# Optimization experiments

Measured on AMD Instinct MI355X. Metric: run time of the kernel, lower is better.

## Reference

```python
import jax, jax.numpy as jnp
import numpy as np

D_MODEL = 2048
B, L = 4, 2048


def _dwconv(x, w, b):
    # x: (B, D, L), w: (D, 1, 3), b: (D,). Causal depthwise conv (PyTorch pad=2 then [...,:L]).
    y = jax.lax.conv_general_dilated(
        x, w, window_strides=(1,), padding=[(2, 0)],
        feature_group_count=x.shape[1], dimension_numbers=("NCH", "OIH", "NCH"))
    return y + b[None, :, None]


def setup_inputs() -> dict:
    key = jax.random.key(0)
    ks = jax.random.split(key, 12)
    D = D_MODEL
    s = 0.02
    inp = {
        "u": jax.random.normal(ks[0], (B, L, D), jnp.float32),
        "Wq": jax.random.normal(ks[1], (D, D), jnp.float32) * s,
        "bq": jnp.zeros((D,), jnp.float32),
        "Wk": jax.random.normal(ks[2], (D, D), jnp.float32) * s,
        "bk": jnp.zeros((D,), jnp.float32),
        "Wv": jax.random.normal(ks[3], (D, D), jnp.float32) * s,
        "bv": jnp.zeros((D,), jnp.float32),
        "convq_w": jax.random.normal(ks[4], (D, 1, 3), jnp.float32) * 0.5,
        "convq_b": jnp.zeros((D,), jnp.float32),
        "convk_w": jax.random.normal(ks[5], (D, 1, 3), jnp.float32) * 0.5,
        "convk_b": jnp.zeros((D,), jnp.float32),
        "ssm_kernel": jax.random.normal(ks[6], (D, L), jnp.float32) * 0.01,  # H = d_model (head_dim=1)
        "D_skip": jax.random.normal(ks[7], (D,), jnp.float32),
        "Wo": jax.random.normal(ks[8], (D, D), jnp.float32) * s,
        "bo": jnp.zeros((D,), jnp.float32),
    }
    return inp


def reference(u, Wq, bq, Wk, bk, Wv, bv, convq_w, convq_b, convk_w, convk_b,
              ssm_kernel, D_skip, Wo, bo):
    # u: (B, L, H)  head_dim = 1 so H == d_model
    Lq = u.shape[1]
    fft_size = 2 * Lq  # L_kernel + L with l_max=None, rate=1

    # q/k/v projections (W @ u.T + b in torch == u @ W.T + b)
    q = jnp.einsum("blh,eh->ble", u, Wq) + bq
    k = jnp.einsum("blh,eh->ble", u, Wk) + bk
    v = jnp.einsum("blh,eh->ble", u, Wv) + bv
    q = jnp.transpose(q, (0, 2, 1))  # (B, H, L)
    k = jnp.transpose(k, (0, 2, 1))
    v = jnp.transpose(v, (0, 2, 1))

    # causal depthwise short convs
    q = _dwconv(q, convq_w, convq_b)
    k = _dwconv(k, convk_w, convk_b)

    # head_dim = 1: kv outer product collapses to elementwise product (B, H, L)
    kv = k * v

    # FFT long convolution: torch does rfft(kv)/n * rfft(kernel), irfft norm='forward'
    # which equals the standard unnormalized circular conv below.
    kv_f = jnp.fft.rfft(kv, n=fft_size)
    kernel_f = jnp.fft.rfft(ssm_kernel, n=fft_size)  # (H, F)
    y = jnp.fft.irfft(kv_f * kernel_f, n=fft_size)[..., :Lq]

    # D skip and q gating
    y = (y + kv * D_skip[None, :, None]) * q  # (B, H, L)

    # output projection
    y = jnp.transpose(y, (0, 2, 1))  # (B, L, H)
    return jnp.einsum("blh,eh->ble", y, Wo) + bo
```

## Files before the change

### kernel.cpp

```cpp
#include <hip/hip_runtime.h>
#include <cstdint>
#include <cstddef>

#define DD 2048
#define LL 2048
#define BB 4
#define MM (BB * LL)
#define NN 6144

typedef __bf16 bf16;
typedef __bf16 bf16x8 __attribute__((ext_vector_type(8)));
typedef __bf16 bf16x4 __attribute__((ext_vector_type(4)));
typedef __bf16 bf16x2 __attribute__((ext_vector_type(2)));
typedef float f32x4 __attribute__((ext_vector_type(4)));

__device__ __forceinline__ void gload16(const void* g, void* l) {
    __builtin_amdgcn_global_load_lds(
        (const __attribute__((address_space(1))) void*)g,
        (__attribute__((address_space(3))) void*)l, 16, 0, 0);
}

__global__ __launch_bounds__(256) void cvt_f32_bf16(const float* __restrict__ s,
                                                    bf16* __restrict__ d, int n8) {
    int i = blockIdx.x * 256 + threadIdx.x;
    if (i >= n8) return;
    const float4* sp = (const float4*)s + (size_t)i * 2;
    float4 a = sp[0], b = sp[1];
    bf16x8 o;
    o[0] = (bf16)a.x; o[1] = (bf16)a.y; o[2] = (bf16)a.z; o[3] = (bf16)a.w;
    o[4] = (bf16)b.x; o[5] = (bf16)b.y; o[6] = (bf16)b.z; o[7] = (bf16)b.w;
    *((bf16x8*)d + i) = o;
}

__device__ __forceinline__ void stage_half(const bf16* g, bf16* l, size_t rstep, int tid) {
    gload16(g, l + tid * 8);
    gload16(g + rstep, l + 4096 + tid * 8);
}

#define MFMA16(J0, J1)                                                         \
    __builtin_amdgcn_s_setprio(1);                                             \
    _Pragma("unroll") for (int i = 0; i < 8; i++)                              \
        acc[i][J0] = __builtin_amdgcn_mfma_f32_16x16x32_bf16(af[i], bq[J0],    \
                                                             acc[i][J0], 0, 0, 0); \
    _Pragma("unroll") for (int i = 0; i < 8; i++)                              \
        acc[i][J1] = __builtin_amdgcn_mfma_f32_16x16x32_bf16(af[i], bq[J1],    \
                                                             acc[i][J1], 0, 0, 0); \
    __builtin_amdgcn_s_setprio(0);

template <int NT>
__device__ __forceinline__ void mma256_loop(const bf16* gA, const bf16* gB,
                                            int Kdim, bf16* lds,
                                            f32x4 (&acc)[8][4]) {
    const int tid = threadIdx.x;
    const int wave = tid >> 6, lane = tid & 63;
    const int wm = wave >> 2, wn = wave & 3;
    const int fm = lane & 15, fg = lane >> 4;
    const size_t rstep = (size_t)128 * Kdim;
    const int koff = ((fg ^ ((fm >> 1) & 3)) << 3);
    const int aoff = (wm * 128 + fm) * 32 + koff;
    const int boff = (wn * 64 + fm) * 32 + koff;

    bf16* const A0 = lds;
    bf16* const B0 = lds + 32768;

#pragma unroll
    for (int i = 0; i < 8; i++)
#pragma unroll
        for (int j = 0; j < 4; j++) acc[i][j] = (f32x4){0.f, 0.f, 0.f, 0.f};

    stage_half(gA, A0, rstep, tid);
    stage_half(gB, B0, rstep, tid);
    stage_half(gA + 32, A0 + 8192, rstep, tid);
    stage_half(gB + 32, B0 + 8192, rstep, tid);

    bf16x8 af[8], bq[4];

    for (int t = 0; t < NT; ++t) {
        const int c = t & 1;
        bf16* const Ac = A0 + c * 16384;
        bf16* const Bc = B0 + c * 16384;
        bf16* const An = A0 + (c ^ 1) * 16384;
        bf16* const Bn = B0 + (c ^ 1) * 16384;
        const bf16* a1 = gA + (t + 1) * 64;
        const bf16* b1 = gB + (t + 1) * 64;
        const bool st = (t + 1 < NT);

        asm volatile("s_waitcnt vmcnt(4)" ::: "memory");
        __builtin_amdgcn_s_barrier();
        if (st) stage_half(a1, An, rstep, tid);
#pragma unroll
        for (int i = 0; i < 8; i++) af[i] = *(const bf16x8*)(Ac + aoff + i * 512);
        bq[0] = *(const bf16x8*)(Bc + boff);
        bq[1] = *(const bf16x8*)(Bc + boff + 512);
        __builtin_amdgcn_s_barrier();
        asm volatile("s_waitcnt lgkmcnt(0)" ::: "memory");
        MFMA16(0, 1)

        __builtin_amdgcn_s_barrier();
        if (st) stage_half(b1, Bn, rstep, tid);
        bq[2] = *(const bf16x8*)(Bc + boff + 1024);
        bq[3] = *(const bf16x8*)(Bc + boff + 1536);
        __builtin_amdgcn_s_barrier();
        asm volatile("s_waitcnt lgkmcnt(0)" ::: "memory");
        MFMA16(2, 3)

        if (st) { asm volatile("s_waitcnt vmcnt(4)" ::: "memory"); }
        else    { asm volatile("s_waitcnt vmcnt(0)" ::: "memory"); }
        __builtin_amdgcn_s_barrier();
        if (st) stage_half(a1 + 32, An + 8192, rstep, tid);
#pragma unroll
        for (int i = 0; i < 8; i++) af[i] = *(const bf16x8*)(Ac + 8192 + aoff + i * 512);
        bq[0] = *(const bf16x8*)(Bc + 8192 + boff);
        bq[1] = *(const bf16x8*)(Bc + 8192 + boff + 512);
        __builtin_amdgcn_s_barrier();
        asm volatile("s_waitcnt lgkmcnt(0)" ::: "memory");
        MFMA16(0, 1)

        __builtin_amdgcn_s_barrier();
        if (st) stage_half(b1 + 32, Bn + 8192, rstep, tid);
        bq[2] = *(const bf16x8*)(Bc + 8192 + boff + 1024);
        bq[3] = *(const bf16x8*)(Bc + 8192 + boff + 1536);
        __builtin_amdgcn_s_barrier();
        asm volatile("s_waitcnt lgkmcnt(0)" ::: "memory");
        MFMA16(2, 3)
    }
}

__global__ __launch_bounds__(512, 2) void gemm_qkv(const bf16* __restrict__ A,
                                                   const bf16* __restrict__ Bm,
                                                   const float* __restrict__ bqp,
                                                   const float* __restrict__ bkp,
                                                   const float* __restrict__ bvp,
                                                   bf16* __restrict__ CtOut) {
    __shared__ bf16 lds[65536];
    const int id = blockIdx.x;
    const int wg = (id & 7) * 96 + (id >> 3);
    const int m0 = (wg & 31) << 8;
    const int n0 = (wg >> 5) << 8;

    const int tid = threadIdx.x;
    const int wave = tid >> 6, lane = tid & 63;
    const int srow = tid >> 2;
    const int skx = (((lane & 3) ^ ((lane >> 3) & 3)) << 3);
    const bf16* gA = A + (size_t)(m0 + srow) * DD + skx;
    const bf16* gB = Bm + (size_t)(n0 + srow) * DD + skx;

    f32x4 acc[8][4];
    mma256_loop<DD / 64>(gA, gB, DD, lds, acc);

    __syncthreads();
    const int wm = wave >> 2, wn = wave & 3;
    const int fm = lane & 15, fg = lane >> 4;
    const float* bp = (n0 < 2048) ? bqp : ((n0 < 4096) ? bkp : bvp);
    const int nb = n0 & 2047;
#pragma unroll
    for (int j = 0; j < 4; j++) {
        const int col = wn * 64 + j * 16 + fm;
        const float bvv = bp[nb + col];
        const int csw = (col & 7) << 3;
#pragma unroll
        for (int i = 0; i < 8; i++) {
            const int row = (wm * 128 + i * 16 + fg * 4) ^ csw;
            bf16x4 o;
#pragma unroll
            for (int r = 0; r < 4; r++) o[r] = (bf16)(acc[i][j][r] + bvv);
            *(bf16x4*)&lds[col * 256 + row] = o;
        }
    }
    __syncthreads();
    const int ccol = tid >> 5, chunk = tid & 31;
#pragma unroll
    for (int p = 0; p < 16; p++) {
        const int col = p * 16 + ccol;
        bf16x8 vv = *(const bf16x8*)&lds[col * 256 + ((chunk * 8) ^ ((col & 7) << 3))];
        *(bf16x8*)(CtOut + (size_t)(n0 + col) * MM + m0 + chunk * 8) = vv;
    }
}

__global__ __launch_bounds__(512, 2) void gemm_bt_f32(const bf16* __restrict__ A,
                                                      const bf16* __restrict__ Bm,
                                                      const float* __restrict__ bias,
                                                      float* __restrict__ C,
                                                      int Ndim, int Kdim) {
    __shared__ bf16 lds[65536];
    const int id = blockIdx.x;
    const int wg = (id & 7) * (gridDim.x >> 3) + (id >> 3);
    const int m0 = (wg & 31) << 8;
    const int n0 = (wg >> 5) << 8;

    const int tid = threadIdx.x;
    const int wave = tid >> 6, lane = tid & 63;
    const int srow = tid >> 2;
    const int skx = (((lane & 3) ^ ((lane >> 3) & 3)) << 3);
    const bf16* gA = A + (size_t)(m0 + srow) * Kdim + skx;
    const bf16* gB = Bm + (size_t)(n0 + srow) * Kdim + skx;

    f32x4 acc[8][4];
    mma256_loop<DD / 64>(gA, gB, Kdim, lds, acc);

    const int wm = wave >> 2, wn = wave & 3;
    const int fm = lane & 15, fg = lane >> 4;
#pragma unroll
    for (int j = 0; j < 4; j++) {
        const int col = n0 + wn * 64 + j * 16 + fm;
        const float bvv = bias[col];
#pragma unroll
        for (int i = 0; i < 8; i++) {
#pragma unroll
            for (int r = 0; r < 4; r++) {
                const int row = m0 + wm * 128 + i * 16 + fg * 4 + r;
                C[(size_t)row * Ndim + col] = acc[i][j][r] + bvv;
            }
        }
    }
}

__global__ __launch_bounds__(256) void dwconv_kv2(
    const bf16* __restrict__ qkvT,
    const float* __restrict__ cqw, const float* __restrict__ cqb,
    const float* __restrict__ ckw, const float* __restrict__ ckb,
    bf16* __restrict__ qcT, bf16* __restrict__ kvT) {
    const int bid = blockIdx.x;
    const int b = bid >> 11, d = bid & (DD - 1);
    const int tid = threadIdx.x;
    const int l = tid * 8;

    const bf16* qR = qkvT + (size_t)d * MM + b * LL;
    const bf16* kR = qkvT + (size_t)(2048 + d) * MM + b * LL;
    const bf16* vR = qkvT + (size_t)(4096 + d) * MM + b * LL;

    const float q0 = cqw[d * 3], q1 = cqw[d * 3 + 1], q2 = cqw[d * 3 + 2];
    const float k0 = ckw[d * 3], k1 = ckw[d * 3 + 1], k2 = ckw[d * 3 + 2];
    const float qb = cqb[d], kb = ckb[d];

    bf16x8 qx = *(const bf16x8*)(qR + l);
    bf16x8 kx = *(const bf16x8*)(kR + l);
    bf16x8 vx = *(const bf16x8*)(vR + l);

    float xq[10], xk[10];
    xq[0] = 0.f; xq[1] = 0.f; xk[0] = 0.f; xk[1] = 0.f;
    if (l >= 2) {
        bf16x2 qh = *(const bf16x2*)(qR + l - 2);
        bf16x2 kh = *(const bf16x2*)(kR + l - 2);
        xq[0] = (float)qh[0]; xq[1] = (float)qh[1];
        xk[0] = (float)kh[0]; xk[1] = (float)kh[1];
    }
#pragma unroll
    for (int c = 0; c < 8; c++) { xq[c + 2] = (float)qx[c]; xk[c + 2] = (float)kx[c]; }

    bf16x8 oq, okv;
#pragma unroll
    for (int c = 0; c < 8; c++) {
        float qc = q0 * xq[c] + q1 * xq[c + 1] + q2 * xq[c + 2] + qb;
        float kc = k0 * xk[c] + k1 * xk[c + 1] + k2 * xk[c + 2] + kb;
        oq[c] = (bf16)qc;
        okv[c] = (bf16)(kc * (float)vx[c]);
    }
    const size_t o = ((size_t)b * DD + d) * LL + l;
    *(bf16x8*)(qcT + o) = oq;
    *(bf16x8*)(kvT + o) = okv;
}

__global__ __launch_bounds__(128, 2) void longconv_gate(
    const bf16* __restrict__ kvT, const bf16* __restrict__ qcT,
    const float* __restrict__ kern, const float* __restrict__ Dskip,
    bf16* __restrict__ ygT) {
    __shared__ bf16 kv_ls[4 * 2112];
    __shared__ float krev_f[2112];
    const int d = blockIdx.x;
    const int tid = threadIdx.x;

    {
        const int bb = tid >> 5, t32 = tid & 31;
#pragma unroll
        for (int c = 0; c < 8; ++c) {
            const int l = (c * 32 + t32) * 8;
            bf16x8 v = *(const bf16x8*)(kvT + ((size_t)bb * DD + d) * LL + l);
            *(bf16x8*)&kv_ls[2112 * bb + 48 + l] = v;
        }
        if (tid < 48) {
#pragma unroll
            for (int b2 = 0; b2 < 4; b2++) kv_ls[2112 * b2 + tid] = (bf16)0.f;
        } else if (tid < 64) {
#pragma unroll
            for (int b2 = 0; b2 < 4; b2++) kv_ls[2112 * b2 + 2048 + tid] = (bf16)0.f;
        }
    }
    {
        const float* kr = kern + (size_t)d * LL;
#pragma unroll
        for (int c = 0; c < 16; ++c) {
            const int x = c * 128 + tid;
            krev_f[x] = kr[2047 - x];
        }
        if (tid < 64) krev_f[2048 + tid] = 0.f;
    }
    __syncthreads();

    const int lane = tid & 63;
    const int w = __builtin_amdgcn_readfirstlane(tid >> 6);
    const int n = lane & 15, q = lane >> 4;
    const int b = n & 3, pp = n >> 2;
    const int cB = 2112 * b + 16 * pp + 8 * q;

    f32x4 acc[16];
#pragma unroll
    for (int s = 0; s < 16; s++) acc[s] = (f32x4){0.f, 0.f, 0.f, 0.f};

    for (int it = 0; it < 64; ++it) {
        const int as = 2031 - 32 * it - n + 8 * q;
        float af[8];
#pragma unroll
        for (int j = 0; j < 8; j++) af[j] = krev_f[as + j];
        bf16x8 a;
#pragma unroll
        for (int j = 0; j < 8; j++) a[j] = (bf16)af[j];

        const int bbase = cB + 64 * w + 32 - 32 * it;
#pragma unroll
        for (int h = 0; h < 2; ++h) {
            bf16x8 bfr[8];
#pragma unroll
            for (int s8 = 0; s8 < 8; s8++) {
                const int s = h * 8 + s8;
                if (it <= 4 * s + 2 * w + 1)
                    bfr[s8] = *(const bf16x8*)&kv_ls[bbase + 128 * s];
            }
#pragma unroll
            for (int s8 = 0; s8 < 8; s8++) {
                const int s = h * 8 + s8;
                if (it <= 4 * s + 2 * w + 1)
                    acc[s] = __builtin_amdgcn_mfma_f32_16x16x32_bf16(
                        a, bfr[s8], acc[s], 0, 0, 0);
            }
        }
    }

    const float dsk = Dskip[d];
#pragma unroll
    for (int s = 0; s < 16; s++) {
        const int i = 2 * s + w;
        const int l = 64 * i + 16 * pp + 4 * q;
        const size_t gb = ((size_t)b * DD + d) * LL + l;
        bf16x4 qc4 = *(const bf16x4*)&qcT[gb];
        bf16x4 kv4 = *(const bf16x4*)&kv_ls[2112 * b + 48 + l];
        bf16x4 o;
#pragma unroll
        for (int r = 0; r < 4; r++) {
            float val = (acc[s][r] + (float)kv4[r] * dsk) * (float)qc4[r];
            o[r] = (bf16)val;
        }
        *(bf16x4*)&ygT[gb] = o;
    }
}

__global__ __launch_bounds__(256) void transpose_dl(const bf16* __restrict__ src,
                                                    bf16* __restrict__ dst) {
    __shared__ bf16 ts[32][33];
    const int b = blockIdx.z;
    const int l0 = blockIdx.x * 32, d0 = blockIdx.y * 32;
    const int tid = threadIdx.x;
    const int c = tid & 31, r0 = tid >> 5;
#pragma unroll
    for (int p = 0; p < 4; p++) {
        int r = r0 + p * 8;
        ts[r][c] = src[((size_t)b * DD + d0 + r) * LL + l0 + c];
    }
    __syncthreads();
#pragma unroll
    for (int p = 0; p < 4; p++) {
        int r = r0 + p * 8;
        dst[((size_t)b * LL + l0 + r) * DD + d0 + c] = ts[c][r];
    }
}

extern "C" void kernel_launch(void* const* d_in, const int* in_sizes, int n_in,
                              void* d_out, int out_size, void* d_ws, size_t ws_size,
                              hipStream_t stream) {
    const float* u   = (const float*)d_in[0];
    const float* Wq  = (const float*)d_in[1];
    const float* bq  = (const float*)d_in[2];
    const float* Wk  = (const float*)d_in[3];
    const float* bk  = (const float*)d_in[4];
    const float* Wv  = (const float*)d_in[5];
    const float* bv  = (const float*)d_in[6];
    const float* cqw = (const float*)d_in[7];
    const float* cqb = (const float*)d_in[8];
    const float* ckw = (const float*)d_in[9];
    const float* ckb = (const float*)d_in[10];
    const float* ssm = (const float*)d_in[11];
    const float* Dsk = (const float*)d_in[12];
    const float* Wo  = (const float*)d_in[13];
    const float* bo  = (const float*)d_in[14];

    char* w = (char*)d_ws;
    bf16* u_bf    = (bf16*)(w);
    bf16* Wqkv_bf = (bf16*)(w + 33554432ull);
    bf16* Wo_bf   = (bf16*)(w + 58720256ull);
    bf16* qkvT    = (bf16*)(w + 67108864ull);
    bf16* qcT     = (bf16*)(w + 167772160ull);
    bf16* kvT     = (bf16*)(w + 201326592ull);

    cvt_f32_bf16<<<8192, 256, 0, stream>>>(u, u_bf, MM * DD / 8);
    cvt_f32_bf16<<<2048, 256, 0, stream>>>(Wq, Wqkv_bf, DD * DD / 8);
    cvt_f32_bf16<<<2048, 256, 0, stream>>>(Wk, Wqkv_bf + 4194304, DD * DD / 8);
    cvt_f32_bf16<<<2048, 256, 0, stream>>>(Wv, Wqkv_bf + 8388608, DD * DD / 8);
    cvt_f32_bf16<<<2048, 256, 0, stream>>>(Wo, Wo_bf, DD * DD / 8);

    gemm_qkv<<<(MM / 256) * (NN / 256), 512, 0, stream>>>(u_bf, Wqkv_bf, bq, bk, bv, qkvT);

    dwconv_kv2<<<BB * DD, 256, 0, stream>>>(qkvT, cqw, cqb, ckw, ckb, qcT, kvT);

    bf16* ygT = u_bf;
    longconv_gate<<<DD, 128, 0, stream>>>(kvT, qcT, ssm, Dsk, ygT);

    bf16* ygTT = qkvT;
    dim3 gc(LL / 32, DD / 32, BB);
    transpose_dl<<<gc, 256, 0, stream>>>(ygT, ygTT);

    gemm_bt_f32<<<(MM / 256) * (DD / 256), 512, 0, stream>>>(ygTT, Wo_bf, bo,
                                                             (float*)d_out, DD, DD);
}
```

Measured before the change: 586.6 us.

## Restructure GEMM MFMA fragment schedule, remap tiles per XCD, widen transpose

The GEMM inner loop now loads A fragments in two groups of four and issues all four B fragments up front, cutting live af registers from 8 to 4 and reordering LDS reads relative to the async stage. Tile-to-block mapping is changed so each XCD owns a contiguous band of 4 M-tiles, to improve L2 reuse of A and B panels. The transpose kernel moves to 64x64 tiles with 16-byte vector loads/stores and an XOR-swizzled LDS layout instead of scalar bf16 accesses. Risks include different LDS bank behavior and that the new mapping assumes specific grid shapes.

```diff
diff --git a/kernel.cpp b/kernel.cpp
--- a/kernel.cpp
+++ b/kernel.cpp
@@ -37,14 +37,12 @@
     gload16(g + rstep, l + 4096 + tid * 8);
 }
 
-#define MFMA16(J0, J1)                                                         \
-    __builtin_amdgcn_s_setprio(1);                                             \
-    _Pragma("unroll") for (int i = 0; i < 8; i++)                              \
-        acc[i][J0] = __builtin_amdgcn_mfma_f32_16x16x32_bf16(af[i], bq[J0],    \
-                                                             acc[i][J0], 0, 0, 0); \
-    _Pragma("unroll") for (int i = 0; i < 8; i++)                              \
-        acc[i][J1] = __builtin_amdgcn_mfma_f32_16x16x32_bf16(af[i], bq[J1],    \
-                                                             acc[i][J1], 0, 0, 0); \
+#define MFMA_BLK(IOFF)                                                          \
+    __builtin_amdgcn_s_setprio(1);                                              \
+    _Pragma("unroll") for (int j = 0; j < 4; j++)                               \
+        _Pragma("unroll") for (int i = 0; i < 4; i++)                           \
+            acc[(IOFF) + i][j] = __builtin_amdgcn_mfma_f32_16x16x32_bf16(       \
+                af[i], bq[j], acc[(IOFF) + i][j], 0, 0, 0);                     \
     __builtin_amdgcn_s_setprio(0);
 
 template <int NT>
@@ -73,7 +71,7 @@
     stage_half(gA + 32, A0 + 8192, rstep, tid);
     stage_half(gB + 32, B0 + 8192, rstep, tid);
 
-    bf16x8 af[8], bq[4];
+    bf16x8 af[4], bq[4];
 
     for (int t = 0; t < NT; ++t) {
         const int c = t & 1;
@@ -87,42 +85,42 @@
 
         asm volatile("s_waitcnt vmcnt(4)" ::: "memory");
         __builtin_amdgcn_s_barrier();
+#pragma unroll
+        for (int i = 0; i < 4; i++) af[i] = *(const bf16x8*)(Ac + aoff + i * 512);
+#pragma unroll
+        for (int j = 0; j < 4; j++) bq[j] = *(const bf16x8*)(Bc + boff + j * 512);
         if (st) stage_half(a1, An, rstep, tid);
-#pragma unroll
-        for (int i = 0; i < 8; i++) af[i] = *(const bf16x8*)(Ac + aoff + i * 512);
-        bq[0] = *(const bf16x8*)(Bc + boff);
-        bq[1] = *(const bf16x8*)(Bc + boff + 512);
         __builtin_amdgcn_s_barrier();
         asm volatile("s_waitcnt lgkmcnt(0)" ::: "memory");
-        MFMA16(0, 1)
-
-        __builtin_amdgcn_s_barrier();
+        MFMA_BLK(0)
+
+        __builtin_amdgcn_s_barrier();
+#pragma unroll
+        for (int i = 0; i < 4; i++) af[i] = *(const bf16x8*)(Ac + aoff + (i + 4) * 512);
         if (st) stage_half(b1, Bn, rstep, tid);
-        bq[2] = *(const bf16x8*)(Bc + boff + 1024);
-        bq[3] = *(const bf16x8*)(Bc + boff + 1536);
         __builtin_amdgcn_s_barrier();
         asm volatile("s_waitcnt lgkmcnt(0)" ::: "memory");
-        MFMA16(2, 3)
+        MFMA_BLK(4)
 
         if (st) { asm volatile("s_waitcnt vmcnt(4)" ::: "memory"); }
         else    { asm volatile("s_waitcnt vmcnt(0)" ::: "memory"); }
         __builtin_amdgcn_s_barrier();
+#pragma unroll
+        for (int i = 0; i < 4; i++) af[i] = *(const bf16x8*)(Ac + 8192 + aoff + i * 512);
+#pragma unroll
+        for (int j = 0; j < 4; j++) bq[j] = *(const bf16x8*)(Bc + 8192 + boff + j * 512);
         if (st) stage_half(a1 + 32, An + 8192, rstep, tid);
-#pragma unroll
-        for (int i = 0; i < 8; i++) af[i] = *(const bf16x8*)(Ac + 8192 + aoff + i * 512);
-        bq[0] = *(const bf16x8*)(Bc + 8192 + boff);
-        bq[1] = *(const bf16x8*)(Bc + 8192 + boff + 512);
         __builtin_amdgcn_s_barrier();
         asm volatile("s_waitcnt lgkmcnt(0)" ::: "memory");
-        MFMA16(0, 1)
-
-        __builtin_amdgcn_s_barrier();
+        MFMA_BLK(0)
+
+        __builtin_amdgcn_s_barrier();
+#pragma unroll
+        for (int i = 0; i < 4; i++) af[i] = *(const bf16x8*)(Ac + 8192 + aoff + (i + 4) * 512);
         if (st) stage_half(b1 + 32, Bn + 8192, rstep, tid);
-        bq[2] = *(const bf16x8*)(Bc + 8192 + boff + 1024);
-        bq[3] = *(const bf16x8*)(Bc + 8192 + boff + 1536);
         __builtin_amdgcn_s_barrier();
         asm volatile("s_waitcnt lgkmcnt(0)" ::: "memory");
-        MFMA16(2, 3)
+        MFMA_BLK(4)
     }
 }
 
@@ -134,9 +132,9 @@
                                                    bf16* __restrict__ CtOut) {
     __shared__ bf16 lds[65536];
     const int id = blockIdx.x;
-    const int wg = (id & 7) * 96 + (id >> 3);
-    const int m0 = (wg & 31) << 8;
-    const int n0 = (wg >> 5) << 8;
+    const int xcd = id & 7, li = id >> 3;
+    const int m0 = (xcd * 4 + (li & 3)) << 8;
+    const int n0 = (li >> 2) << 8;
 
     const int tid = threadIdx.x;
     const int wave = tid >> 6, lane = tid & 63;
@@ -184,9 +182,9 @@
                                                       int Ndim, int Kdim) {
     __shared__ bf16 lds[65536];
     const int id = blockIdx.x;
-    const int wg = (id & 7) * (gridDim.x >> 3) + (id >> 3);
-    const int m0 = (wg & 31) << 8;
-    const int n0 = (wg >> 5) << 8;
+    const int xcd = id & 7, li = id >> 3;
+    const int m0 = (xcd * 4 + (li & 3)) << 8;
+    const int n0 = (li >> 2) << 8;
 
     const int tid = threadIdx.x;
     const int wave = tid >> 6, lane = tid & 63;
@@ -356,21 +354,31 @@
 
 __global__ __launch_bounds__(256) void transpose_dl(const bf16* __restrict__ src,
                                                     bf16* __restrict__ dst) {
-    __shared__ bf16 ts[32][33];
+    __shared__ bf16 ts[64 * 64];
     const int b = blockIdx.z;
-    const int l0 = blockIdx.x * 32, d0 = blockIdx.y * 32;
-    const int tid = threadIdx.x;
-    const int c = tid & 31, r0 = tid >> 5;
-#pragma unroll
-    for (int p = 0; p < 4; p++) {
-        int r = r0 + p * 8;
-        ts[r][c] = src[((size_t)b * DD + d0 + r) * LL + l0 + c];
+    const int l0 = blockIdx.x * 64, d0 = blockIdx.y * 64;
+    const int tid = threadIdx.x;
+    {
+        const int r0 = tid >> 3, c8 = tid & 7;
+#pragma unroll
+        for (int h = 0; h < 2; h++) {
+            const int r = r0 + h * 32;
+            bf16x8 v = *(const bf16x8*)&src[((size_t)b * DD + d0 + r) * LL + l0 + c8 * 8];
+            *(bf16x8*)&ts[r * 64 + ((c8 ^ (r & 7)) << 3)] = v;
+        }
     }
     __syncthreads();
-#pragma unroll
-    for (int p = 0; p < 4; p++) {
-        int r = r0 + p * 8;
-        dst[((size_t)b * LL + l0 + r) * DD + d0 + c] = ts[c][r];
+    const int l = tid & 63, dc0 = (tid >> 6) << 3;
+#pragma unroll
+    for (int half = 0; half < 2; half++) {
+        const int dc = dc0 + half * 32;
+        bf16x8 o;
+#pragma unroll
+        for (int j = 0; j < 8; j++) {
+            const int r = dc + j;
+            o[j] = ts[r * 64 + (((l >> 3) ^ (r & 7)) << 3) + (l & 7)];
+        }
+        *(bf16x8*)&dst[((size_t)b * LL + l0 + l) * DD + d0 + dc] = o;
     }
 }
 
@@ -415,7 +423,7 @@
     longconv_gate<<<DD, 128, 0, stream>>>(kvT, qcT, ssm, Dsk, ygT);
 
     bf16* ygTT = qkvT;
-    dim3 gc(LL / 32, DD / 32, BB);
+    dim3 gc(LL / 64, DD / 64, BB);
     transpose_dl<<<gc, 256, 0, stream>>>(ygT, ygTT);
 
     gemm_bt_f32<<<(MM / 256) * (DD / 256), 512, 0, stream>>>(ygTT, Wo_bf, bo,
```

Measured after the change: 578.2 us. No clear change (-1.4%).
